# Kernel optimization log

Hardware: AMD Instinct MI355X
Metric: run time of the kernel (lower is better)

## Reference

```python
import jax, jax.numpy as jnp
import numpy as np

HEADS = 8
HEAD_DIM = 64
IN_DIM = HEADS * HEAD_DIM  # 512
SCALE = HEAD_DIM ** (-0.5)


def _split_heads(t):
    # [b, n, h*d] -> [b, h, n, d]
    b, n, _ = t.shape
    return t.reshape(b, n, HEADS, HEAD_DIM).transpose(0, 2, 1, 3)


def _merge_heads(t):
    # [b, h, n, d] -> [b, n, h*d]
    b, h, n, d = t.shape
    return t.transpose(0, 2, 1, 3).reshape(b, n, h * d)


def setup_inputs() -> dict:
    key = jax.random.key(0)
    ks = jax.random.split(key, 6)
    b, n = 8, 1024
    nv = jax.random.normal(ks[0], (b, n, IN_DIM), dtype=jnp.float32)
    rv = jax.random.normal(ks[1], (b, n, IN_DIM), dtype=jnp.float32)
    s = IN_DIM ** (-0.5)
    W_noise = jax.random.normal(ks[2], (IN_DIM, 2 * IN_DIM), dtype=jnp.float32) * s
    b_noise = jnp.zeros((2 * IN_DIM,), dtype=jnp.float32)
    W_rgb = jax.random.normal(ks[3], (IN_DIM, 2 * IN_DIM), dtype=jnp.float32) * s
    b_rgb = jnp.zeros((2 * IN_DIM,), dtype=jnp.float32)
    return {"nv": nv, "rv": rv, "W_noise": W_noise, "b_noise": b_noise,
            "W_rgb": W_rgb, "b_rgb": b_rgb}


def reference(nv, rv, W_noise, b_noise, W_rgb, b_rgb):
    # qk projections, chunk(2, dim=-1)
    nqk = nv @ W_noise + b_noise                      # [b, n, 2*in_dim]
    noise_q, noise_k = jnp.split(nqk, 2, axis=-1)
    rqk = rv @ W_rgb + b_rgb
    rgb_q, rgb_k = jnp.split(rqk, 2, axis=-1)

    noise_q, noise_k = _split_heads(noise_q), _split_heads(noise_k)  # [b,h,n,d]
    rgb_q, rgb_k = _split_heads(rgb_q), _split_heads(rgb_k)

    attn1 = jnp.einsum('bhnd,bhmd->bhnm', noise_q, rgb_k) * SCALE
    attn2 = jnp.einsum('bhnd,bhmd->bhnm', rgb_q, noise_k) * SCALE

    # NOTE: original uses nn.Softmax(dim=1) => softmax over the HEADS axis.
    attn1 = jax.nn.softmax(attn1, axis=1)
    attn2 = jax.nn.softmax(attn2, axis=1)

    rv_h = _split_heads(rv)  # values are the raw inputs, not projections
    nv_h = _split_heads(nv)

    noise = jnp.einsum('bhnm,bhmd->bhnd', attn1, rv_h)
    rgb = jnp.einsum('bhnm,bhmd->bhnd', attn2, nv_h)

    return (_merge_heads(noise), _merge_heads(rgb))
```

## Files before the change

### kernel.cpp

```cpp
#include <hip/hip_runtime.h>
#include <hip/hip_bf16.h>

typedef __attribute__((ext_vector_type(8))) short short8;
typedef __attribute__((ext_vector_type(4))) short short4v;
typedef __attribute__((ext_vector_type(4))) float float4v;

#define MFMA16(a, b, c) __builtin_amdgcn_mfma_f32_16x16x32_bf16(a, b, c, 0, 0, 0)

__device__ __forceinline__ short f2bf(float f) {
    __hip_bfloat16 hb = __float2bfloat16(f);
    return *reinterpret_cast<short*>(&hb);
}

__global__ __launch_bounds__(256) void wt_kernel(
    const float* __restrict__ Wn, const float* __restrict__ Wr,
    __hip_bfloat16* __restrict__ Wtn, __hip_bfloat16* __restrict__ Wtr)
{
    const int c0 = blockIdx.x * 64;
    const int k0 = blockIdx.y * 64;
    const int g  = blockIdx.z;
    const float* W = g ? Wr : Wn;
    __hip_bfloat16* Wt = g ? Wtr : Wtn;

    __shared__ short lds[64][72];
    const int t = threadIdx.x;
    {
        const int i  = t >> 2;
        const int j0 = (t & 3) * 16;
        const float* p = W + (size_t)(k0 + i) * 1024 + c0 + j0;
        #pragma unroll
        for (int jj = 0; jj < 16; ++jj)
            lds[j0 + jj][i] = f2bf(p[jj]);
    }
    __syncthreads();
    {
        const int j  = t >> 2;
        const int i0 = (t & 3) * 16;
        __hip_bfloat16* q = Wt + (size_t)(c0 + j) * 512 + k0 + i0;
        short8 v0 = *reinterpret_cast<const short8*>(&lds[j][i0]);
        short8 v1 = *reinterpret_cast<const short8*>(&lds[j][i0 + 8]);
        *reinterpret_cast<short8*>(q)     = v0;
        *reinterpret_cast<short8*>(q + 8) = v1;
    }
}

__global__ __launch_bounds__(256) void prep_kernel(
    const float* __restrict__ nv, const float* __restrict__ rv,
    __hip_bfloat16* __restrict__ Vtn, __hip_bfloat16* __restrict__ Vtr,
    __hip_bfloat16* __restrict__ An,  __hip_bfloat16* __restrict__ Ar)
{
    const int ntile = blockIdx.x & 15;
    const int src   = blockIdx.x >> 4;
    const int h     = blockIdx.y;
    const int b     = blockIdx.z;
    const float* V  = src ? rv : nv;
    __hip_bfloat16* Vt = src ? Vtr : Vtn;
    __hip_bfloat16* Ab = src ? Ar  : An;

    __shared__ short lds[64][72];
    const int t  = threadIdx.x;
    const int n0 = ntile * 64;
    {
        const int i  = t >> 2;
        const int j0 = (t & 3) * 16;
        const float* p = V + ((size_t)(b * 1024) + n0 + i) * 512 + h * 64 + j0;
        short8 a0, a1;
        #pragma unroll
        for (int jj = 0; jj < 8; ++jj) {
            short x = f2bf(p[jj]);
            a0[jj] = x; lds[j0 + jj][i] = x;
        }
        #pragma unroll
        for (int jj = 0; jj < 8; ++jj) {
            short x = f2bf(p[8 + jj]);
            a1[jj] = x; lds[j0 + 8 + jj][i] = x;
        }
        __hip_bfloat16* adst = Ab + ((size_t)(b * 1024) + n0 + i) * 512 + h * 64 + j0;
        *reinterpret_cast<short8*>(adst)     = a0;
        *reinterpret_cast<short8*>(adst + 8) = a1;
    }
    __syncthreads();
    {
        const int j  = t >> 2;
        const int i0 = (t & 3) * 16;
        __hip_bfloat16* q = Vt + (((size_t)(b * 8 + h) * 64) + j) * 1024 + n0 + i0;
        short8 v0 = *reinterpret_cast<const short8*>(&lds[j][i0]);
        short8 v1 = *reinterpret_cast<const short8*>(&lds[j][i0 + 8]);
        *reinterpret_cast<short8*>(q)     = v0;
        *reinterpret_cast<short8*>(q + 8) = v1;
    }
}

__global__ __launch_bounds__(256, 4) void proj_kernel(
    const __hip_bfloat16* __restrict__ An, const __hip_bfloat16* __restrict__ Ar,
    const __hip_bfloat16* __restrict__ Wtn, const __hip_bfloat16* __restrict__ Wtr,
    const float* __restrict__ bn, const float* __restrict__ br,
    __hip_bfloat16* __restrict__ Qn, __hip_bfloat16* __restrict__ Kn,
    __hip_bfloat16* __restrict__ Qr, __hip_bfloat16* __restrict__ Kr)
{
    const int m0 = blockIdx.x * 64;
    const int c0 = blockIdx.y * 256;
    const int g  = blockIdx.z;
    const __hip_bfloat16* A  = g ? Ar  : An;
    const __hip_bfloat16* Wt = g ? Wtr : Wtn;
    const float* bias = g ? br : bn;
    __hip_bfloat16* Qd = g ? Qr : Qn;
    __hip_bfloat16* Kd = g ? Kr : Kn;

    __shared__ short Bt[2][4][256][8];

    const int t    = threadIdx.x;
    const int lane = t & 63;
    const int w    = t >> 6;
    const int l15  = lane & 15;
    const int lg   = lane >> 4;

    auto stage = [&](int buf, int kk) {
        #pragma unroll
        for (int rep = 0; rep < 4; ++rep) {
            const int u = rep * 256 + t;
            const int s = u >> 8;
            const int c = u & 255;
            const __hip_bfloat16* src = Wt + (size_t)(c0 + c) * 512 + kk + s * 8;
            __builtin_amdgcn_global_load_lds(
                (const __attribute__((address_space(1))) unsigned int*)src,
                (__attribute__((address_space(3))) unsigned int*)&Bt[buf][s][c][0],
                16, 0, 0);
        }
    };

    float4v acc[16] = {};
    const int mrow = m0 + w * 16 + l15;

    stage(0, 0);
    __syncthreads();

    for (int kk = 0; kk < 512; kk += 32) {
        const int buf = (kk >> 5) & 1;
        if (kk < 480) stage(buf ^ 1, kk + 32);
        short8 afrag = *reinterpret_cast<const short8*>(
            A + (size_t)mrow * 512 + kk + lg * 8);
        #pragma unroll
        for (int cs = 0; cs < 16; ++cs) {
            short8 bfrag = *reinterpret_cast<const short8*>(
                &Bt[buf][lg][cs * 16 + l15][0]);
            acc[cs] = MFMA16(afrag, bfrag, acc[cs]);
        }
        __syncthreads();
    }

    #pragma unroll
    for (int cs = 0; cs < 16; ++cs) {
        const int c  = c0 + cs * 16 + l15;
        const bool isK = (c >= 512);
        const int hh = (c >> 6) & 7;
        const int d  = c & 63;
        __hip_bfloat16* dst = isK ? Kd : Qd;
        const float bv = bias[c];
        #pragma unroll
        for (int r = 0; r < 4; ++r) {
            const int m = m0 + w * 16 + lg * 4 + r;
            const int b = m >> 10, n = m & 1023;
            dst[(((size_t)(b * 8 + hh) * 1024 + n) * 64) + d] =
                __float2bfloat16(acc[cs][r] + bv);
        }
    }
}

__global__ __launch_bounds__(512, 2) void attn_kernel(
    const __hip_bfloat16* __restrict__ Qn, const __hip_bfloat16* __restrict__ Kn,
    const __hip_bfloat16* __restrict__ Qr, const __hip_bfloat16* __restrict__ Kr,
    const __hip_bfloat16* __restrict__ Vtn, const __hip_bfloat16* __restrict__ Vtr,
    float* __restrict__ out)
{
    const int combo = blockIdx.x;
    const int bb    = combo & 7;
    const int dir   = combo >> 3;
    const int nt    = blockIdx.y;
    const __hip_bfloat16* Q  = dir ? Qr  : Qn;
    const __hip_bfloat16* K  = dir ? Kn  : Kr;
    const __hip_bfloat16* Vt = dir ? Vtn : Vtr;
    float* O = out + (size_t)dir * (8u * 1024u * 512u);

    const int t    = threadIdx.x;
    const int lane = t & 63;
    const int w    = t >> 6;
    const int iw   = w & 1;
    const int hg   = w >> 1;
    const int h0   = hg * 2;
    const int l15  = lane & 15;
    const int lg   = lane >> 4;

    __shared__ short K_s[2][8 * 32 * 64];
    __shared__ short P_s[8][32][40];
    __shared__ float X_s[2][4][2][512];

    const int n0 = nt * 64;
    const float C = 0.125f * 1.44269504f;

    const __hip_bfloat16* Vb[2] = {
        Vt + (size_t)((bb * 8 + h0)     * 64) * 1024,
        Vt + (size_t)((bb * 8 + h0 + 1) * 64) * 1024 };

    auto stage = [&](int bufn, int mt) {
        #pragma unroll
        for (int i = 0; i < 4; ++i) {
            const int u    = (w * 4 + i) * 64 + lane;
            const int h    = u >> 8;
            const int mr   = (u >> 3) & 31;
            const int slot = (u & 7) ^ (mr & 7);
            const __hip_bfloat16* g =
                K + ((size_t)((bb * 8 + h) * 1024) + mt + mr) * 64 + slot * 8;
            __builtin_amdgcn_global_load_lds(
                (const __attribute__((address_space(1))) unsigned int*)g,
                (__attribute__((address_space(3))) unsigned int*)&K_s[bufn][u * 8],
                16, 0, 0);
        }
    };

    short8 qf[2][2][2];
    #pragma unroll
    for (int ns = 0; ns < 2; ++ns)
        #pragma unroll
        for (int hh = 0; hh < 2; ++hh)
            #pragma unroll
            for (int kc = 0; kc < 2; ++kc)
                qf[ns][hh][kc] = *reinterpret_cast<const short8*>(
                    Q + ((size_t)((bb * 8 + h0 + hh) * 1024) + n0 + ns * 32 + iw * 16 + l15) * 64
                      + kc * 32 + lg * 8);

    float4v oacc[2][2][4] = {};

    stage(0, 0);
    __syncthreads();

    for (int it = 0; it < 32; ++it) {
        const int m0  = it << 5;
        const int buf = it & 1;
        short8 vf[2][4];
        #pragma unroll
        for (int hh = 0; hh < 2; ++hh)
            #pragma unroll
            for (int dd = 0; dd < 4; ++dd)
                vf[hh][dd] = *reinterpret_cast<const short8*>(
                    Vb[hh] + (size_t)(dd * 16 + l15) * 1024 + m0 + lg * 8);
        short8 kf[2][2][2];
        const short* ks = K_s[buf];
        #pragma unroll
        for (int hh = 0; hh < 2; ++hh)
            #pragma unroll
            for (int j = 0; j < 2; ++j) {
                const int mr = j * 16 + l15;
                #pragma unroll
                for (int kc = 0; kc < 2; ++kc)
                    kf[hh][j][kc] = *reinterpret_cast<const short8*>(
                        ks + (h0 + hh) * 2048 + mr * 64
                           + (((kc * 4 + lg) ^ (mr & 7)) * 8));
            }

        #pragma unroll
        for (int ns = 0; ns < 2; ++ns) {
            float4v sacc[2][2] = {};
            #pragma unroll
            for (int hh = 0; hh < 2; ++hh)
                #pragma unroll
                for (int j = 0; j < 2; ++j)
                    #pragma unroll
                    for (int kc = 0; kc < 2; ++kc)
                        sacc[hh][j] = MFMA16(kf[hh][j][kc], qf[ns][hh][kc], sacc[hh][j]);
            float e[2][8];
            float ps[8] = {0.f, 0.f, 0.f, 0.f, 0.f, 0.f, 0.f, 0.f};
            #pragma unroll
            for (int hh = 0; hh < 2; ++hh)
                #pragma unroll
                for (int j = 0; j < 2; ++j)
                    #pragma unroll
                    for (int r = 0; r < 4; ++r) {
                        float ev = exp2f(sacc[hh][j][r] * C);
                        e[hh][j * 4 + r] = ev;
                        ps[j * 4 + r] += ev;
                    }
            #pragma unroll
            for (int p = 0; p < 8; ++p)
                X_s[ns][hg][iw][p * 64 + lane] = ps[p];
            __syncthreads();
            if (ns == 0)
                stage(buf ^ 1, (it < 31) ? m0 + 32 : 0);
            float inv[8];
            #pragma unroll
            for (int p = 0; p < 8; ++p) {
                float tot = ps[p];
                #pragma unroll
                for (int g = 1; g < 4; ++g)
                    tot += X_s[ns][(hg + g) & 3][iw][p * 64 + lane];
                inv[p] = __builtin_amdgcn_rcpf(tot);
            }
            #pragma unroll
            for (int hh = 0; hh < 2; ++hh)
                #pragma unroll
                for (int j = 0; j < 2; ++j) {
                    short4v pk;
                    #pragma unroll
                    for (int r = 0; r < 4; ++r)
                        pk[r] = f2bf(e[hh][j * 4 + r] * inv[j * 4 + r]);
                    *reinterpret_cast<short4v*>(
                        &P_s[h0 + hh][iw * 16 + l15][j * 16 + lg * 4]) = pk;
                }
            #pragma unroll
            for (int hh = 0; hh < 2; ++hh) {
                short8 pf = *reinterpret_cast<const short8*>(
                    &P_s[h0 + hh][iw * 16 + l15][lg * 8]);
                #pragma unroll
                for (int dd = 0; dd < 4; ++dd)
                    oacc[ns][hh][dd] = MFMA16(pf, vf[hh][dd], oacc[ns][hh][dd]);
            }
        }
        __syncthreads();
    }

    #pragma unroll
    for (int ns = 0; ns < 2; ++ns)
        #pragma unroll
        for (int hh = 0; hh < 2; ++hh)
            #pragma unroll
            for (int dd = 0; dd < 4; ++dd)
                #pragma unroll
                for (int r = 0; r < 4; ++r) {
                    const int n = n0 + ns * 32 + iw * 16 + lg * 4 + r;
                    const int d = dd * 16 + l15;
                    O[((size_t)(bb * 1024) + n) * 512 + (h0 + hh) * 64 + d] =
                        oacc[ns][hh][dd][r];
                }
}

extern "C" void kernel_launch(void* const* d_in, const int* in_sizes, int n_in,
                              void* d_out, int out_size, void* d_ws, size_t ws_size,
                              hipStream_t stream) {
    const float* nv = (const float*)d_in[0];
    const float* rv = (const float*)d_in[1];
    const float* Wn = (const float*)d_in[2];
    const float* bn = (const float*)d_in[3];
    const float* Wr = (const float*)d_in[4];
    const float* br = (const float*)d_in[5];
    float* out = (float*)d_out;

    __hip_bfloat16* w = (__hip_bfloat16*)d_ws;
    const size_t E = 8ull * 8 * 1024 * 64;
    __hip_bfloat16* Qn  = w;
    __hip_bfloat16* Kn  = w + E;
    __hip_bfloat16* Qr  = w + 2 * E;
    __hip_bfloat16* Kr  = w + 3 * E;
    __hip_bfloat16* Vtn = w + 4 * E;
    __hip_bfloat16* Vtr = w + 5 * E;
    __hip_bfloat16* An  = w + 6 * E;
    __hip_bfloat16* Ar  = w + 7 * E;
    __hip_bfloat16* Wtn = w + 8 * E;
    __hip_bfloat16* Wtr = w + 8 * E + 512 * 1024;

    wt_kernel  <<<dim3(16, 8, 2), 256, 0, stream>>>(Wn, Wr, Wtn, Wtr);
    prep_kernel<<<dim3(32, 8, 8), 256, 0, stream>>>(nv, rv, Vtn, Vtr, An, Ar);
    proj_kernel<<<dim3(128, 4, 2), 256, 0, stream>>>(An, Ar, Wtn, Wtr, bn, br,
                                                     Qn, Kn, Qr, Kr);
    attn_kernel<<<dim3(16, 16), 512, 0, stream>>>(Qn, Kn, Qr, Kr, Vtn, Vtr, out);
}
```

Before: 172.1 us.

## Fold weight transpose into prep kernel and single-buffer K tile in attention

The weight-transpose kernel becomes an extra z-slice of the prep kernel, which removes one kernel launch. The attention kernel drops its double-buffered K shared-memory tile for a single buffer and raises its launch bounds minimum blocks per CU from 2 to 4, aiming for less LDS use and higher occupancy. The attention grid has only 256 blocks, so extra occupancy may not be usable. The tighter register budget risks spills, and the single buffer gives up overlap between K prefetch and compute.

New measurement: 170.2 us. No clear change (-1.1%).

```diff
diff --git a/kernel.cpp b/kernel.cpp
--- a/kernel.cpp
+++ b/kernel.cpp
@@ -12,43 +12,44 @@
     return *reinterpret_cast<short*>(&hb);
 }
 
-__global__ __launch_bounds__(256) void wt_kernel(
+__global__ __launch_bounds__(256) void prep_kernel(
+    const float* __restrict__ nv, const float* __restrict__ rv,
     const float* __restrict__ Wn, const float* __restrict__ Wr,
+    __hip_bfloat16* __restrict__ Vtn, __hip_bfloat16* __restrict__ Vtr,
+    __hip_bfloat16* __restrict__ An,  __hip_bfloat16* __restrict__ Ar,
     __hip_bfloat16* __restrict__ Wtn, __hip_bfloat16* __restrict__ Wtr)
 {
-    const int c0 = blockIdx.x * 64;
-    const int k0 = blockIdx.y * 64;
-    const int g  = blockIdx.z;
-    const float* W = g ? Wr : Wn;
-    __hip_bfloat16* Wt = g ? Wtr : Wtn;
-
     __shared__ short lds[64][72];
     const int t = threadIdx.x;
-    {
-        const int i  = t >> 2;
-        const int j0 = (t & 3) * 16;
-        const float* p = W + (size_t)(k0 + i) * 1024 + c0 + j0;
-        #pragma unroll
-        for (int jj = 0; jj < 16; ++jj)
-            lds[j0 + jj][i] = f2bf(p[jj]);
-    }
-    __syncthreads();
-    {
-        const int j  = t >> 2;
-        const int i0 = (t & 3) * 16;
-        __hip_bfloat16* q = Wt + (size_t)(c0 + j) * 512 + k0 + i0;
-        short8 v0 = *reinterpret_cast<const short8*>(&lds[j][i0]);
-        short8 v1 = *reinterpret_cast<const short8*>(&lds[j][i0 + 8]);
-        *reinterpret_cast<short8*>(q)     = v0;
-        *reinterpret_cast<short8*>(q + 8) = v1;
-    }
-}
-
-__global__ __launch_bounds__(256) void prep_kernel(
-    const float* __restrict__ nv, const float* __restrict__ rv,
-    __hip_bfloat16* __restrict__ Vtn, __hip_bfloat16* __restrict__ Vtr,
-    __hip_bfloat16* __restrict__ An,  __hip_bfloat16* __restrict__ Ar)
-{
+
+    if (blockIdx.z == 8) {
+        const int id = blockIdx.x + 32 * blockIdx.y;
+        const int c0 = (id & 15) * 64;
+        const int k0 = ((id >> 4) & 7) * 64;
+        const int g  = id >> 7;
+        const float* W = g ? Wr : Wn;
+        __hip_bfloat16* Wt = g ? Wtr : Wtn;
+        {
+            const int i  = t >> 2;
+            const int j0 = (t & 3) * 16;
+            const float* p = W + (size_t)(k0 + i) * 1024 + c0 + j0;
+            #pragma unroll
+            for (int jj = 0; jj < 16; ++jj)
+                lds[j0 + jj][i] = f2bf(p[jj]);
+        }
+        __syncthreads();
+        {
+            const int j  = t >> 2;
+            const int i0 = (t & 3) * 16;
+            __hip_bfloat16* q = Wt + (size_t)(c0 + j) * 512 + k0 + i0;
+            short8 v0 = *reinterpret_cast<const short8*>(&lds[j][i0]);
+            short8 v1 = *reinterpret_cast<const short8*>(&lds[j][i0 + 8]);
+            *reinterpret_cast<short8*>(q)     = v0;
+            *reinterpret_cast<short8*>(q + 8) = v1;
+        }
+        return;
+    }
+
     const int ntile = blockIdx.x & 15;
     const int src   = blockIdx.x >> 4;
     const int h     = blockIdx.y;
@@ -57,8 +58,6 @@
     __hip_bfloat16* Vt = src ? Vtr : Vtn;
     __hip_bfloat16* Ab = src ? Ar  : An;
 
-    __shared__ short lds[64][72];
-    const int t  = threadIdx.x;
     const int n0 = ntile * 64;
     {
         const int i  = t >> 2;
@@ -167,7 +166,7 @@
     }
 }
 
-__global__ __launch_bounds__(512, 2) void attn_kernel(
+__global__ __launch_bounds__(512, 4) void attn_kernel(
     const __hip_bfloat16* __restrict__ Qn, const __hip_bfloat16* __restrict__ Kn,
     const __hip_bfloat16* __restrict__ Qr, const __hip_bfloat16* __restrict__ Kr,
     const __hip_bfloat16* __restrict__ Vtn, const __hip_bfloat16* __restrict__ Vtr,
@@ -191,7 +190,7 @@
     const int l15  = lane & 15;
     const int lg   = lane >> 4;
 
-    __shared__ short K_s[2][8 * 32 * 64];
+    __shared__ short K_s[8 * 32 * 64];
     __shared__ short P_s[8][32][40];
     __shared__ float X_s[2][4][2][512];
 
@@ -202,7 +201,7 @@
         Vt + (size_t)((bb * 8 + h0)     * 64) * 1024,
         Vt + (size_t)((bb * 8 + h0 + 1) * 64) * 1024 };
 
-    auto stage = [&](int bufn, int mt) {
+    auto stage = [&](int mt) {
         #pragma unroll
         for (int i = 0; i < 4; ++i) {
             const int u    = (w * 4 + i) * 64 + lane;
@@ -213,7 +212,7 @@
                 K + ((size_t)((bb * 8 + h) * 1024) + mt + mr) * 64 + slot * 8;
             __builtin_amdgcn_global_load_lds(
                 (const __attribute__((address_space(1))) unsigned int*)g,
-                (__attribute__((address_space(3))) unsigned int*)&K_s[bufn][u * 8],
+                (__attribute__((address_space(3))) unsigned int*)&K_s[u * 8],
                 16, 0, 0);
         }
     };
@@ -231,12 +230,11 @@
 
     float4v oacc[2][2][4] = {};
 
-    stage(0, 0);
+    stage(0);
     __syncthreads();
 
     for (int it = 0; it < 32; ++it) {
-        const int m0  = it << 5;
-        const int buf = it & 1;
+        const int m0 = it << 5;
         short8 vf[2][4];
         #pragma unroll
         for (int hh = 0; hh < 2; ++hh)
@@ -245,7 +243,6 @@
                 vf[hh][dd] = *reinterpret_cast<const short8*>(
                     Vb[hh] + (size_t)(dd * 16 + l15) * 1024 + m0 + lg * 8);
         short8 kf[2][2][2];
-        const short* ks = K_s[buf];
         #pragma unroll
         for (int hh = 0; hh < 2; ++hh)
             #pragma unroll
@@ -254,8 +251,8 @@
                 #pragma unroll
                 for (int kc = 0; kc < 2; ++kc)
                     kf[hh][j][kc] = *reinterpret_cast<const short8*>(
-                        ks + (h0 + hh) * 2048 + mr * 64
-                           + (((kc * 4 + lg) ^ (mr & 7)) * 8));
+                        K_s + (h0 + hh) * 2048 + mr * 64
+                            + (((kc * 4 + lg) ^ (mr & 7)) * 8));
             }
 
         #pragma unroll
@@ -285,7 +282,7 @@
                 X_s[ns][hg][iw][p * 64 + lane] = ps[p];
             __syncthreads();
             if (ns == 0)
-                stage(buf ^ 1, (it < 31) ? m0 + 32 : 0);
+                stage((it < 31) ? m0 + 32 : 0);
             float inv[8];
             #pragma unroll
             for (int p = 0; p < 8; ++p) {
@@ -357,8 +354,8 @@
     __hip_bfloat16* Wtn = w + 8 * E;
     __hip_bfloat16* Wtr = w + 8 * E + 512 * 1024;
 
-    wt_kernel  <<<dim3(16, 8, 2), 256, 0, stream>>>(Wn, Wr, Wtn, Wtr);
-    prep_kernel<<<dim3(32, 8, 8), 256, 0, stream>>>(nv, rv, Vtn, Vtr, An, Ar);
+    prep_kernel<<<dim3(32, 8, 9), 256, 0, stream>>>(nv, rv, Wn, Wr,
+                                                    Vtn, Vtr, An, Ar, Wtn, Wtr);
     proj_kernel<<<dim3(128, 4, 2), 256, 0, stream>>>(An, Ar, Wtn, Wtr, bn, br,
                                                      Qn, Kn, Qr, Kr);
     attn_kernel<<<dim3(16, 16), 512, 0, stream>>>(Qn, Kn, Qr, Kr, Vtn, Vtr, out);
```

## Merge weight transpose into prep kernel and read fp32 activations directly in projection

Applied to the files above, without the earlier changes.

Folds the weight transpose/convert kernel into the prep kernel as an extra grid slice, removing one launch. The projection kernel now loads fp32 activations and converts them to bf16 in registers, so the bf16 activation copies are no longer written and re-read. In exchange, the projection reads twice as many activation bytes per k-step, and each A fragment is re-read across the four column blocks in fp32.

After: 169.7 us. No clear change (-1.4%).

```diff
diff --git a/kernel.cpp b/kernel.cpp
--- a/kernel.cpp
+++ b/kernel.cpp
@@ -12,72 +12,58 @@
     return *reinterpret_cast<short*>(&hb);
 }
 
-__global__ __launch_bounds__(256) void wt_kernel(
+__global__ __launch_bounds__(256) void prep_kernel(
+    const float* __restrict__ nv, const float* __restrict__ rv,
     const float* __restrict__ Wn, const float* __restrict__ Wr,
+    __hip_bfloat16* __restrict__ Vtn, __hip_bfloat16* __restrict__ Vtr,
     __hip_bfloat16* __restrict__ Wtn, __hip_bfloat16* __restrict__ Wtr)
 {
-    const int c0 = blockIdx.x * 64;
-    const int k0 = blockIdx.y * 64;
-    const int g  = blockIdx.z;
-    const float* W = g ? Wr : Wn;
-    __hip_bfloat16* Wt = g ? Wtr : Wtn;
-
     __shared__ short lds[64][72];
     const int t = threadIdx.x;
-    {
-        const int i  = t >> 2;
-        const int j0 = (t & 3) * 16;
-        const float* p = W + (size_t)(k0 + i) * 1024 + c0 + j0;
-        #pragma unroll
-        for (int jj = 0; jj < 16; ++jj)
-            lds[j0 + jj][i] = f2bf(p[jj]);
-    }
-    __syncthreads();
-    {
-        const int j  = t >> 2;
-        const int i0 = (t & 3) * 16;
-        __hip_bfloat16* q = Wt + (size_t)(c0 + j) * 512 + k0 + i0;
-        short8 v0 = *reinterpret_cast<const short8*>(&lds[j][i0]);
-        short8 v1 = *reinterpret_cast<const short8*>(&lds[j][i0 + 8]);
-        *reinterpret_cast<short8*>(q)     = v0;
-        *reinterpret_cast<short8*>(q + 8) = v1;
-    }
-}
-
-__global__ __launch_bounds__(256) void prep_kernel(
-    const float* __restrict__ nv, const float* __restrict__ rv,
-    __hip_bfloat16* __restrict__ Vtn, __hip_bfloat16* __restrict__ Vtr,
-    __hip_bfloat16* __restrict__ An,  __hip_bfloat16* __restrict__ Ar)
-{
+
+    if (blockIdx.z == 8) {
+        const int id = blockIdx.x + 32 * blockIdx.y;
+        const int c0 = (id & 15) * 64;
+        const int k0 = ((id >> 4) & 7) * 64;
+        const int g  = id >> 7;
+        const float* W = g ? Wr : Wn;
+        __hip_bfloat16* Wt = g ? Wtr : Wtn;
+        {
+            const int i  = t >> 2;
+            const int j0 = (t & 3) * 16;
+            const float* p = W + (size_t)(k0 + i) * 1024 + c0 + j0;
+            #pragma unroll
+            for (int jj = 0; jj < 16; ++jj)
+                lds[j0 + jj][i] = f2bf(p[jj]);
+        }
+        __syncthreads();
+        {
+            const int j  = t >> 2;
+            const int i0 = (t & 3) * 16;
+            __hip_bfloat16* q = Wt + (size_t)(c0 + j) * 512 + k0 + i0;
+            short8 v0 = *reinterpret_cast<const short8*>(&lds[j][i0]);
+            short8 v1 = *reinterpret_cast<const short8*>(&lds[j][i0 + 8]);
+            *reinterpret_cast<short8*>(q)     = v0;
+            *reinterpret_cast<short8*>(q + 8) = v1;
+        }
+        return;
+    }
+
     const int ntile = blockIdx.x & 15;
     const int src   = blockIdx.x >> 4;
     const int h     = blockIdx.y;
     const int b     = blockIdx.z;
     const float* V  = src ? rv : nv;
     __hip_bfloat16* Vt = src ? Vtr : Vtn;
-    __hip_bfloat16* Ab = src ? Ar  : An;
-
-    __shared__ short lds[64][72];
-    const int t  = threadIdx.x;
+
     const int n0 = ntile * 64;
     {
         const int i  = t >> 2;
         const int j0 = (t & 3) * 16;
         const float* p = V + ((size_t)(b * 1024) + n0 + i) * 512 + h * 64 + j0;
-        short8 a0, a1;
-        #pragma unroll
-        for (int jj = 0; jj < 8; ++jj) {
-            short x = f2bf(p[jj]);
-            a0[jj] = x; lds[j0 + jj][i] = x;
-        }
-        #pragma unroll
-        for (int jj = 0; jj < 8; ++jj) {
-            short x = f2bf(p[8 + jj]);
-            a1[jj] = x; lds[j0 + 8 + jj][i] = x;
-        }
-        __hip_bfloat16* adst = Ab + ((size_t)(b * 1024) + n0 + i) * 512 + h * 64 + j0;
-        *reinterpret_cast<short8*>(adst)     = a0;
-        *reinterpret_cast<short8*>(adst + 8) = a1;
+        #pragma unroll
+        for (int jj = 0; jj < 16; ++jj)
+            lds[j0 + jj][i] = f2bf(p[jj]);
     }
     __syncthreads();
     {
@@ -92,7 +78,7 @@
 }
 
 __global__ __launch_bounds__(256, 4) void proj_kernel(
-    const __hip_bfloat16* __restrict__ An, const __hip_bfloat16* __restrict__ Ar,
+    const float* __restrict__ nv, const float* __restrict__ rv,
     const __hip_bfloat16* __restrict__ Wtn, const __hip_bfloat16* __restrict__ Wtr,
     const float* __restrict__ bn, const float* __restrict__ br,
     __hip_bfloat16* __restrict__ Qn, __hip_bfloat16* __restrict__ Kn,
@@ -101,7 +87,7 @@
     const int m0 = blockIdx.x * 64;
     const int c0 = blockIdx.y * 256;
     const int g  = blockIdx.z;
-    const __hip_bfloat16* A  = g ? Ar  : An;
+    const float* A = g ? rv : nv;
     const __hip_bfloat16* Wt = g ? Wtr : Wtn;
     const float* bias = g ? br : bn;
     __hip_bfloat16* Qd = g ? Qr : Qn;
@@ -138,8 +124,15 @@
     for (int kk = 0; kk < 512; kk += 32) {
         const int buf = (kk >> 5) & 1;
         if (kk < 480) stage(buf ^ 1, kk + 32);
-        short8 afrag = *reinterpret_cast<const short8*>(
-            A + (size_t)mrow * 512 + kk + lg * 8);
+        short8 afrag;
+        {
+            const float* ap = A + (size_t)mrow * 512 + kk + lg * 8;
+            float4 a0 = *reinterpret_cast<const float4*>(ap);
+            float4 a1 = *reinterpret_cast<const float4*>(ap + 4);
+            short* af = (short*)&afrag;
+            af[0] = f2bf(a0.x); af[1] = f2bf(a0.y); af[2] = f2bf(a0.z); af[3] = f2bf(a0.w);
+            af[4] = f2bf(a1.x); af[5] = f2bf(a1.y); af[6] = f2bf(a1.z); af[7] = f2bf(a1.w);
+        }
         #pragma unroll
         for (int cs = 0; cs < 16; ++cs) {
             short8 bfrag = *reinterpret_cast<const short8*>(
@@ -352,14 +345,12 @@
     __hip_bfloat16* Kr  = w + 3 * E;
     __hip_bfloat16* Vtn = w + 4 * E;
     __hip_bfloat16* Vtr = w + 5 * E;
-    __hip_bfloat16* An  = w + 6 * E;
-    __hip_bfloat16* Ar  = w + 7 * E;
-    __hip_bfloat16* Wtn = w + 8 * E;
-    __hip_bfloat16* Wtr = w + 8 * E + 512 * 1024;
-
-    wt_kernel  <<<dim3(16, 8, 2), 256, 0, stream>>>(Wn, Wr, Wtn, Wtr);
-    prep_kernel<<<dim3(32, 8, 8), 256, 0, stream>>>(nv, rv, Vtn, Vtr, An, Ar);
-    proj_kernel<<<dim3(128, 4, 2), 256, 0, stream>>>(An, Ar, Wtn, Wtr, bn, br,
+    __hip_bfloat16* Wtn = w + 6 * E;
+    __hip_bfloat16* Wtr = w + 6 * E + 512 * 1024;
+
+    prep_kernel<<<dim3(32, 8, 9), 256, 0, stream>>>(nv, rv, Wn, Wr,
+                                                    Vtn, Vtr, Wtn, Wtr);
+    proj_kernel<<<dim3(128, 4, 2), 256, 0, stream>>>(nv, rv, Wtn, Wtr, bn, br,
                                                      Qn, Kn, Qr, Kr);
     attn_kernel<<<dim3(16, 16), 512, 0, stream>>>(Qn, Kn, Qr, Kr, Vtn, Vtr, out);
 }
```
